# Optimization experiments

Measured on AMD Instinct MI355X. Metric: run time of the kernel, lower is better.

The kernel has to match this reference:

```python
import jax, jax.numpy as jnp
import numpy as np

B, C, L, H = 8, 1024, 1024, 16
DK = C // H
SCALE = 1.0 / np.sqrt(DK)


def setup_inputs() -> dict:
    key = jax.random.key(0)
    ks = jax.random.split(key, 9)
    s = 1.0 / np.sqrt(C)
    return {
        "q": jax.random.normal(ks[0], (B, C, L), dtype=jnp.float32),
        "k": jax.random.normal(ks[1], (B, C, L), dtype=jnp.float32),
        "v": jax.random.normal(ks[2], (B, C, L), dtype=jnp.float32),
        "Wq": jax.random.normal(ks[3], (C, C), dtype=jnp.float32) * s,
        "bq": jax.random.normal(ks[4], (C,), dtype=jnp.float32) * s,
        "Wk": jax.random.normal(ks[5], (C, C), dtype=jnp.float32) * s,
        "bk": jax.random.normal(ks[6], (C,), dtype=jnp.float32) * s,
        "Wv": jax.random.normal(ks[7], (C, C), dtype=jnp.float32) * s,
        "bv": jax.random.normal(ks[8], (C,), dtype=jnp.float32) * s,
    }


def _proj(x, W, b):
    # Conv1d kernel_size=1 == pointwise linear over channels: (b,c,l) -> (b,o,l)
    return jnp.einsum('oc,bcl->bol', W, x) + b[None, :, None]


def reference(q, k, v, Wq, bq, Wk, bk, Wv, bv):
    b = q.shape[0]
    qh = _proj(q, Wq, bq).reshape(b * H, DK, L)
    kh = _proj(k, Wk, bk).reshape(b * H, DK, L)
    vh = _proj(v, Wv, bv).reshape(b * H, DK, L)
    # scores[bh, t, s] = sum_c q[bh,c,t] k[bh,c,s]
    scores = jnp.einsum('bct,bcs->bts', qh, kh) * SCALE
    # NOTE: original uses nn.Softmax(dim=1) -> softmax over the query axis t
    attn = jax.nn.softmax(scores, axis=1)
    # dropout is identity in eval / p=0
    out = jnp.einsum('bts,bcs->bct', attn, vh)  # (b*H, d_k, L)
    return out.reshape(b, C, L)
```

## Files before the change

### kernel.cpp

```cpp
#include <hip/hip_runtime.h>
#include <stdint.h>

typedef unsigned short ushort_t;
typedef float  f32x4  __attribute__((ext_vector_type(4)));
typedef short  short8 __attribute__((ext_vector_type(8)));
typedef short  short4v __attribute__((ext_vector_type(4)));

#define QSCALE 0.18033688011112043f

__device__ __forceinline__ ushort_t f2bf(float f) {
  unsigned u = __builtin_bit_cast(unsigned, f);
  unsigned r = (u + 0x7fffu + ((u >> 16) & 1u)) >> 16;
  return (ushort_t)r;
}
__device__ __forceinline__ float bf2f(ushort_t u) {
  unsigned x = (unsigned)u << 16;
  return __builtin_bit_cast(float, x);
}

typedef const __attribute__((address_space(1))) unsigned int* gas_t;
typedef __attribute__((address_space(3))) unsigned int* las_t;
__device__ __forceinline__ void gload16(const void* g, void* l) {
  __builtin_amdgcn_global_load_lds((gas_t)g, (las_t)l, 16, 0, 0);
}

__global__ __launch_bounds__(256) void transpose_cvt3(
    const float* __restrict__ q, const float* __restrict__ k,
    const float* __restrict__ v, ushort_t* __restrict__ oq,
    ushort_t* __restrict__ ok, ushort_t* __restrict__ ov) {
  __shared__ float tile[64][65];
  int z = blockIdx.z;
  int t = z >> 3, b = z & 7;
  const float* in = (t == 0) ? q : (t == 1) ? k : v;
  ushort_t* out = (t == 0) ? oq : (t == 1) ? ok : ov;
  int c0 = blockIdx.x * 64, l0 = blockIdx.y * 64;
  int col = threadIdx.x & 63;
  int row4 = threadIdx.x >> 6;
  const float* p = in + ((size_t)b * 1024 + c0) * 1024 + l0;
#pragma unroll
  for (int i = 0; i < 16; ++i) {
    int r = row4 * 16 + i;
    tile[r][col] = p[(size_t)r * 1024 + col];
  }
  __syncthreads();
  ushort_t* qo = out + ((size_t)b * 1024 + l0) * 1024 + c0;
#pragma unroll
  for (int i = 0; i < 16; ++i) {
    int r = row4 * 16 + i;
    qo[(size_t)r * 1024 + col] = f2bf(tile[col][r]);
  }
}

__global__ __launch_bounds__(256) void cvt_w3(
    const float* __restrict__ Wq, const float* __restrict__ Wk,
    const float* __restrict__ Wv, ushort_t* __restrict__ oq,
    ushort_t* __restrict__ ok, ushort_t* __restrict__ ov) {
  int seg = blockIdx.x >> 10;
  const float* in = (seg == 0) ? Wq : (seg == 1) ? Wk : Wv;
  ushort_t* out = (seg == 0) ? oq : (seg == 1) ? ok : ov;
  float sc = (seg == 0) ? QSCALE : 1.0f;
  int i = (blockIdx.x & 1023) * 256 + threadIdx.x;
  f32x4 v = *reinterpret_cast<const f32x4*>(in + (size_t)i * 4);
  short4v pk;
#pragma unroll
  for (int j = 0; j < 4; ++j) pk[j] = (short)f2bf(v[j] * sc);
  *reinterpret_cast<short4v*>(out + (size_t)i * 4) = pk;
}

template <bool OUT_T>
__global__ __launch_bounds__(256) void gemm_bt(const ushort_t* __restrict__ A,
                                               const ushort_t* __restrict__ BT,
                                               const float* __restrict__ bias,
                                               float bs,
                                               ushort_t* __restrict__ outp) {
  __shared__ ushort_t As[128 * 32];
  __shared__ ushort_t Bs[128 * 32];
  int b = blockIdx.z;
  int Mbase = blockIdx.y * 128, Nbase = blockIdx.x * 128;
  int tid = threadIdx.x;
  int lane = tid & 63, wave = tid >> 6;
  int wr = wave >> 1, wc = wave & 1;
  int lo = lane & 15, hi = lane >> 4;
  const ushort_t* Bb = BT + ((size_t)b << 20);

  f32x4 acc[4][4] = {};

  for (int kt = 0; kt < 1024; kt += 32) {
#pragma unroll
    for (int it = 0; it < 2; ++it) {
      int cch = tid + it * 256;
      int r = cch >> 2, p = cch & 3;
      gload16(A + (size_t)(Mbase + r) * 1024 + kt + p * 8, &As[it * 2048 + wave * 512]);
      gload16(Bb + (size_t)(Nbase + r) * 1024 + kt + p * 8, &Bs[it * 2048 + wave * 512]);
    }
    __syncthreads();
    short8 af[4], bf[4];
#pragma unroll
    for (int m = 0; m < 4; ++m)
      af[m] = *reinterpret_cast<const short8*>(&As[(wr * 64 + m * 16 + lo) * 32 + hi * 8]);
#pragma unroll
    for (int n = 0; n < 4; ++n)
      bf[n] = *reinterpret_cast<const short8*>(&Bs[(wc * 64 + n * 16 + lo) * 32 + hi * 8]);
#pragma unroll
    for (int m = 0; m < 4; ++m)
#pragma unroll
      for (int n = 0; n < 4; ++n)
        acc[m][n] = __builtin_amdgcn_mfma_f32_16x16x32_bf16(af[m], bf[n], acc[m][n], 0, 0, 0);
    __syncthreads();
  }

#pragma unroll
  for (int m = 0; m < 4; ++m) {
    int o0 = Mbase + wr * 64 + m * 16 + hi * 4;
#pragma unroll
    for (int n = 0; n < 4; ++n) {
      int col = Nbase + wc * 64 + n * 16 + lo;
      if (OUT_T) {
        short4v pk;
#pragma unroll
        for (int j = 0; j < 4; ++j) pk[j] = (short)f2bf(acc[m][n][j] + bias[o0 + j] * bs);
        *reinterpret_cast<short4v*>(outp + ((size_t)b << 20) + ((size_t)(o0 >> 6) << 16) +
                                    (size_t)col * 64 + (o0 & 63)) = pk;
      } else {
#pragma unroll
        for (int j = 0; j < 4; ++j)
          outp[((size_t)b << 20) + (size_t)(o0 + j) * 1024 + col] =
              f2bf(acc[m][n][j] + bias[o0 + j] * bs);
      }
    }
  }
}

__global__ __launch_bounds__(256) void attn_zs(const ushort_t* __restrict__ qhT,
                                               const ushort_t* __restrict__ khT,
                                               ushort_t* __restrict__ vhb) {
  __shared__ float zbuf[2][2][64];
  __shared__ float invs[128];
  int bid = blockIdx.y * 8 + blockIdx.x;
  int logical = (bid & 7) * 128 + (bid >> 3);
  int sblk = logical & 7, bh = logical >> 3;
  int tid = threadIdx.x;
  int lane = tid & 63, wave = tid >> 6;
  int wr = wave >> 1, wc = wave & 1;
  int lo = lane & 15, hi = lane >> 4;
  const ushort_t* kb = khT + ((size_t)bh << 16);
  const ushort_t* qb = qhT + ((size_t)bh << 16);

  int sbase = sblk * 128 + wr * 64;
  short8 af[4][2];
#pragma unroll
  for (int m = 0; m < 4; ++m)
#pragma unroll
    for (int kk = 0; kk < 2; ++kk)
      af[m][kk] = *reinterpret_cast<const short8*>(
          kb + (size_t)(sbase + m * 16 + lo) * 64 + kk * 32 + hi * 8);

  float zp[4][4] = {};

  for (int t0 = 0; t0 < 1024; t0 += 128) {
    int tbase = t0 + wc * 64;
    short8 bf[4][2];
#pragma unroll
    for (int n = 0; n < 4; ++n)
#pragma unroll
      for (int kk = 0; kk < 2; ++kk)
        bf[n][kk] = *reinterpret_cast<const short8*>(
            qb + (size_t)(tbase + n * 16 + lo) * 64 + kk * 32 + hi * 8);
#pragma unroll
    for (int m = 0; m < 4; ++m)
#pragma unroll
      for (int n = 0; n < 4; ++n) {
        f32x4 dd = {0.f, 0.f, 0.f, 0.f};
        __builtin_amdgcn_s_setprio(1);
        dd = __builtin_amdgcn_mfma_f32_16x16x32_bf16(af[m][0], bf[n][0], dd, 0, 0, 0);
        dd = __builtin_amdgcn_mfma_f32_16x16x32_bf16(af[m][1], bf[n][1], dd, 0, 0, 0);
        __builtin_amdgcn_s_setprio(0);
#pragma unroll
        for (int j = 0; j < 4; ++j) zp[m][j] += __builtin_amdgcn_exp2f(dd[j]);
      }
  }
#pragma unroll
  for (int m = 0; m < 4; ++m)
#pragma unroll
    for (int j = 0; j < 4; ++j) {
      float v = zp[m][j];
      v += __shfl_xor(v, 1);
      v += __shfl_xor(v, 2);
      v += __shfl_xor(v, 4);
      v += __shfl_xor(v, 8);
      if (lo == 0) zbuf[wc][wr][m * 16 + hi * 4 + j] = v;
    }
  __syncthreads();
  if (tid < 128)
    invs[tid] = 1.0f / (zbuf[0][tid >> 6][tid & 63] + zbuf[1][tid >> 6][tid & 63]);
  __syncthreads();

  int d = tid >> 2, soff = (tid & 3) * 32;
  ushort_t* vp = vhb + ((size_t)bh << 16) + (size_t)d * 1024 + sblk * 128 + soff;
#pragma unroll
  for (int c = 0; c < 4; ++c) {
    short8 vv = *reinterpret_cast<const short8*>(vp + c * 8);
    short8 o;
#pragma unroll
    for (int j = 0; j < 8; ++j)
      o[j] = (short)f2bf(bf2f((ushort_t)vv[j]) * invs[soff + c * 8 + j]);
    *reinterpret_cast<short8*>(vp + c * 8) = o;
  }
}

__global__ __launch_bounds__(256) void attn_av(const ushort_t* __restrict__ qhT,
                                               const ushort_t* __restrict__ khT,
                                               const ushort_t* __restrict__ vs,
                                               float* __restrict__ out) {
  __shared__ ushort_t Ks[2][64 * 64];
  __shared__ ushort_t Vt[2][64 * 64];
  __shared__ ushort_t Pt[4][32 * 64];
  int bid = blockIdx.y * 8 + blockIdx.x;
  int logical = (bid & 7) * 128 + (bid >> 3);
  int tblk = logical & 7, bh = logical >> 3;
  int tid = threadIdx.x;
  int lane = tid & 63, wave = tid >> 6;
  int lo = lane & 15, hi = lane >> 4;
  const ushort_t* qb = qhT + ((size_t)bh << 16);
  const char* kbase = (const char*)(khT + ((size_t)bh << 16));
  const char* vbase = (const char*)(vs + ((size_t)bh << 16));
  int t0 = tblk * 128 + wave * 32;

  short8 bq[2][2];
#pragma unroll
  for (int n = 0; n < 2; ++n)
#pragma unroll
    for (int kk = 0; kk < 2; ++kk)
      bq[n][kk] = *reinterpret_cast<const short8*>(
          qb + (size_t)(t0 + n * 16 + lo) * 64 + kk * 32 + hi * 8);

  f32x4 acc[4][2] = {};
  char* pw = (char*)Pt[wave];
  int swl = (lo & 7) << 4;

  auto stageKV = [&](int buf, int s0) {
#pragma unroll
    for (int r = 0; r < 2; ++r) {
      int L = r * 4096 + tid * 16;
      int row = L >> 7;
      int off = (L & 127) ^ ((row & 7) << 4);
      gload16(kbase + (size_t)(s0 + row) * 128 + off,
              (char*)Ks + buf * 8192 + r * 4096 + wave * 1024);
      gload16(vbase + (size_t)row * 2048 + (size_t)s0 * 2 + off,
              (char*)Vt + buf * 8192 + r * 4096 + wave * 1024);
    }
  };

  auto computeTile = [&](int buf) {
    char* ksb = (char*)Ks + buf * 8192;
    char* vtb = (char*)Vt + buf * 8192;
#pragma unroll
    for (int m = 0; m < 4; ++m) {
      int srow = m * 16 + lo;
      int sws = (srow & 7) << 4;
      short8 af0 = *reinterpret_cast<const short8*>(ksb + srow * 128 + ((hi * 16) ^ sws));
      short8 af1 = *reinterpret_cast<const short8*>(ksb + srow * 128 + ((64 + hi * 16) ^ sws));
#pragma unroll
      for (int n = 0; n < 2; ++n) {
        f32x4 dd = {0.f, 0.f, 0.f, 0.f};
        __builtin_amdgcn_s_setprio(1);
        dd = __builtin_amdgcn_mfma_f32_16x16x32_bf16(af0, bq[n][0], dd, 0, 0, 0);
        dd = __builtin_amdgcn_mfma_f32_16x16x32_bf16(af1, bq[n][1], dd, 0, 0, 0);
        __builtin_amdgcn_s_setprio(0);
        short4v pk;
#pragma unroll
        for (int j = 0; j < 4; ++j) pk[j] = (short)f2bf(__builtin_amdgcn_exp2f(dd[j]));
        *reinterpret_cast<short4v*>(
            pw + (n * 16 + lo) * 128 + ((m * 32 + hi * 8) ^ swl)) = pk;
      }
    }
    asm volatile("s_waitcnt lgkmcnt(0)" ::: "memory");
    __builtin_amdgcn_sched_barrier(0);

    short8 bp[2][2];
#pragma unroll
    for (int n = 0; n < 2; ++n)
#pragma unroll
      for (int kk = 0; kk < 2; ++kk)
        bp[n][kk] = *reinterpret_cast<const short8*>(
            pw + (n * 16 + lo) * 128 + ((kk * 64 + hi * 16) ^ swl));
    __builtin_amdgcn_s_setprio(1);
#pragma unroll
    for (int m = 0; m < 4; ++m) {
      int drow = m * 16 + lo;
      int swd = (drow & 7) << 4;
      short8 av0 = *reinterpret_cast<const short8*>(vtb + drow * 128 + ((hi * 16) ^ swd));
      short8 av1 = *reinterpret_cast<const short8*>(vtb + drow * 128 + ((64 + hi * 16) ^ swd));
#pragma unroll
      for (int n = 0; n < 2; ++n) {
        acc[m][n] = __builtin_amdgcn_mfma_f32_16x16x32_bf16(av0, bp[n][0], acc[m][n], 0, 0, 0);
        acc[m][n] = __builtin_amdgcn_mfma_f32_16x16x32_bf16(av1, bp[n][1], acc[m][n], 0, 0, 0);
      }
    }
    __builtin_amdgcn_s_setprio(0);
  };

  stageKV(0, 0);
#pragma unroll 1
  for (int i = 0; i < 15; ++i) {
    stageKV((i + 1) & 1, (i + 1) * 64);
    asm volatile("s_waitcnt vmcnt(4)" ::: "memory");
    __builtin_amdgcn_s_barrier();
    __builtin_amdgcn_sched_barrier(0);
    computeTile(i & 1);
    __builtin_amdgcn_s_barrier();
  }
  asm volatile("s_waitcnt vmcnt(0)" ::: "memory");
  __builtin_amdgcn_s_barrier();
  __builtin_amdgcn_sched_barrier(0);
  computeTile(1);

  float* ob = out + ((size_t)bh << 16);
#pragma unroll
  for (int m = 0; m < 4; ++m)
#pragma unroll
    for (int n = 0; n < 2; ++n)
#pragma unroll
      for (int j = 0; j < 4; ++j)
        ob[(size_t)(m * 16 + hi * 4 + j) * 1024 + t0 + n * 16 + lo] = acc[m][n][j];
}

extern "C" void kernel_launch(void* const* d_in, const int* in_sizes, int n_in,
                              void* d_out, int out_size, void* d_ws, size_t ws_size,
                              hipStream_t stream) {
  const float* q  = (const float*)d_in[0];
  const float* k  = (const float*)d_in[1];
  const float* v  = (const float*)d_in[2];
  const float* Wq = (const float*)d_in[3];
  const float* bq = (const float*)d_in[4];
  const float* Wk = (const float*)d_in[5];
  const float* bk = (const float*)d_in[6];
  const float* Wv = (const float*)d_in[7];
  const float* bv = (const float*)d_in[8];
  float* out = (float*)d_out;
  char* ws = (char*)d_ws;
  const size_t MB = 1u << 20;

  ushort_t* xTq = (ushort_t*)(ws);
  ushort_t* xTk = (ushort_t*)(ws + 16 * MB);
  ushort_t* xTv = (ushort_t*)(ws + 32 * MB);
  ushort_t* Wqb = (ushort_t*)(ws + 48 * MB);
  ushort_t* Wkb = (ushort_t*)(ws + 50 * MB);
  ushort_t* Wvb = (ushort_t*)(ws + 52 * MB);
  ushort_t* qhT = (ushort_t*)(ws + 54 * MB);
  ushort_t* khT = xTq;
  ushort_t* vhb = xTk;

  dim3 tb(256);
  transpose_cvt3<<<dim3(16, 16, 24), tb, 0, stream>>>(q, k, v, xTq, xTk, xTv);
  cvt_w3<<<dim3(3072), tb, 0, stream>>>(Wq, Wk, Wv, Wqb, Wkb, Wvb);
  gemm_bt<true ><<<dim3(8, 8, 8), tb, 0, stream>>>(Wqb, xTq, bq, QSCALE, qhT);
  gemm_bt<true ><<<dim3(8, 8, 8), tb, 0, stream>>>(Wkb, xTk, bk, 1.0f, khT);
  gemm_bt<false><<<dim3(8, 8, 8), tb, 0, stream>>>(Wvb, xTv, bv, 1.0f, vhb);
  attn_zs<<<dim3(8, 128), tb, 0, stream>>>(qhT, khT, vhb);
  attn_av<<<dim3(8, 128), tb, 0, stream>>>(qhT, khT, vhb, out);
}
```

Before: 333.6 us.

## Remap GEMM grid to 1D batch-interleaved, drop setprio and KV double-buffering

The projection GEMMs now launch as a flat 1D grid whose block index is decoded so consecutive blocks land on different batches. The attention kernels drop the s_setprio hints around MFMA groups. attn_av replaces its double-buffered K/V staging, with explicit vmcnt waits and barriers, by a single-buffer load, __syncthreads, compute, __syncthreads loop. This halves shared memory, which may allow more resident blocks, but the global loads no longer overlap with compute.

```diff
diff --git a/kernel.cpp b/kernel.cpp
--- a/kernel.cpp
+++ b/kernel.cpp
@@ -75,8 +75,10 @@
                                                ushort_t* __restrict__ outp) {
   __shared__ ushort_t As[128 * 32];
   __shared__ ushort_t Bs[128 * 32];
-  int b = blockIdx.z;
-  int Mbase = blockIdx.y * 128, Nbase = blockIdx.x * 128;
+  int bid = blockIdx.x;
+  int b = bid & 7;
+  int within = bid >> 3;
+  int Mbase = (within >> 3) * 128, Nbase = (within & 7) * 128;
   int tid = threadIdx.x;
   int lane = tid & 63, wave = tid >> 6;
   int wr = wave >> 1, wc = wave & 1;
@@ -171,10 +173,8 @@
 #pragma unroll
       for (int n = 0; n < 4; ++n) {
         f32x4 dd = {0.f, 0.f, 0.f, 0.f};
-        __builtin_amdgcn_s_setprio(1);
         dd = __builtin_amdgcn_mfma_f32_16x16x32_bf16(af[m][0], bf[n][0], dd, 0, 0, 0);
         dd = __builtin_amdgcn_mfma_f32_16x16x32_bf16(af[m][1], bf[n][1], dd, 0, 0, 0);
-        __builtin_amdgcn_s_setprio(0);
 #pragma unroll
         for (int j = 0; j < 4; ++j) zp[m][j] += __builtin_amdgcn_exp2f(dd[j]);
       }
@@ -212,8 +212,8 @@
                                                const ushort_t* __restrict__ khT,
                                                const ushort_t* __restrict__ vs,
                                                float* __restrict__ out) {
-  __shared__ ushort_t Ks[2][64 * 64];
-  __shared__ ushort_t Vt[2][64 * 64];
+  __shared__ ushort_t Ks[64 * 64];
+  __shared__ ushort_t Vt[64 * 64];
   __shared__ ushort_t Pt[4][32 * 64];
   int bid = blockIdx.y * 8 + blockIdx.x;
   int logical = (bid & 7) * 128 + (bid >> 3);
@@ -238,35 +238,32 @@
   char* pw = (char*)Pt[wave];
   int swl = (lo & 7) << 4;
 
-  auto stageKV = [&](int buf, int s0) {
+  for (int s0 = 0; s0 < 1024; s0 += 64) {
 #pragma unroll
     for (int r = 0; r < 2; ++r) {
       int L = r * 4096 + tid * 16;
       int row = L >> 7;
       int off = (L & 127) ^ ((row & 7) << 4);
       gload16(kbase + (size_t)(s0 + row) * 128 + off,
-              (char*)Ks + buf * 8192 + r * 4096 + wave * 1024);
+              (char*)Ks + r * 4096 + wave * 1024);
       gload16(vbase + (size_t)row * 2048 + (size_t)s0 * 2 + off,
-              (char*)Vt + buf * 8192 + r * 4096 + wave * 1024);
-    }
-  };
-
-  auto computeTile = [&](int buf) {
-    char* ksb = (char*)Ks + buf * 8192;
-    char* vtb = (char*)Vt + buf * 8192;
+              (char*)Vt + r * 4096 + wave * 1024);
+    }
+    __syncthreads();
+
 #pragma unroll
     for (int m = 0; m < 4; ++m) {
       int srow = m * 16 + lo;
       int sws = (srow & 7) << 4;
-      short8 af0 = *reinterpret_cast<const short8*>(ksb + srow * 128 + ((hi * 16) ^ sws));
-      short8 af1 = *reinterpret_cast<const short8*>(ksb + srow * 128 + ((64 + hi * 16) ^ sws));
+      short8 af0 = *reinterpret_cast<const short8*>(
+          (char*)Ks + srow * 128 + ((hi * 16) ^ sws));
+      short8 af1 = *reinterpret_cast<const short8*>(
+          (char*)Ks + srow * 128 + ((64 + hi * 16) ^ sws));
 #pragma unroll
       for (int n = 0; n < 2; ++n) {
         f32x4 dd = {0.f, 0.f, 0.f, 0.f};
-        __builtin_amdgcn_s_setprio(1);
         dd = __builtin_amdgcn_mfma_f32_16x16x32_bf16(af0, bq[n][0], dd, 0, 0, 0);
         dd = __builtin_amdgcn_mfma_f32_16x16x32_bf16(af1, bq[n][1], dd, 0, 0, 0);
-        __builtin_amdgcn_s_setprio(0);
         short4v pk;
 #pragma unroll
         for (int j = 0; j < 4; ++j) pk[j] = (short)f2bf(__builtin_amdgcn_exp2f(dd[j]));
@@ -284,36 +281,22 @@
       for (int kk = 0; kk < 2; ++kk)
         bp[n][kk] = *reinterpret_cast<const short8*>(
             pw + (n * 16 + lo) * 128 + ((kk * 64 + hi * 16) ^ swl));
-    __builtin_amdgcn_s_setprio(1);
 #pragma unroll
     for (int m = 0; m < 4; ++m) {
       int drow = m * 16 + lo;
       int swd = (drow & 7) << 4;
-      short8 av0 = *reinterpret_cast<const short8*>(vtb + drow * 128 + ((hi * 16) ^ swd));
-      short8 av1 = *reinterpret_cast<const short8*>(vtb + drow * 128 + ((64 + hi * 16) ^ swd));
+      short8 av0 = *reinterpret_cast<const short8*>(
+          (char*)Vt + drow * 128 + ((hi * 16) ^ swd));
+      short8 av1 = *reinterpret_cast<const short8*>(
+          (char*)Vt + drow * 128 + ((64 + hi * 16) ^ swd));
 #pragma unroll
       for (int n = 0; n < 2; ++n) {
         acc[m][n] = __builtin_amdgcn_mfma_f32_16x16x32_bf16(av0, bp[n][0], acc[m][n], 0, 0, 0);
         acc[m][n] = __builtin_amdgcn_mfma_f32_16x16x32_bf16(av1, bp[n][1], acc[m][n], 0, 0, 0);
       }
     }
-    __builtin_amdgcn_s_setprio(0);
-  };
-
-  stageKV(0, 0);
-#pragma unroll 1
-  for (int i = 0; i < 15; ++i) {
-    stageKV((i + 1) & 1, (i + 1) * 64);
-    asm volatile("s_waitcnt vmcnt(4)" ::: "memory");
-    __builtin_amdgcn_s_barrier();
-    __builtin_amdgcn_sched_barrier(0);
-    computeTile(i & 1);
-    __builtin_amdgcn_s_barrier();
-  }
-  asm volatile("s_waitcnt vmcnt(0)" ::: "memory");
-  __builtin_amdgcn_s_barrier();
-  __builtin_amdgcn_sched_barrier(0);
-  computeTile(1);
+    __syncthreads();
+  }
 
   float* ob = out + ((size_t)bh << 16);
 #pragma unroll
@@ -354,9 +337,9 @@
   dim3 tb(256);
   transpose_cvt3<<<dim3(16, 16, 24), tb, 0, stream>>>(q, k, v, xTq, xTk, xTv);
   cvt_w3<<<dim3(3072), tb, 0, stream>>>(Wq, Wk, Wv, Wqb, Wkb, Wvb);
-  gemm_bt<true ><<<dim3(8, 8, 8), tb, 0, stream>>>(Wqb, xTq, bq, QSCALE, qhT);
-  gemm_bt<true ><<<dim3(8, 8, 8), tb, 0, stream>>>(Wkb, xTk, bk, 1.0f, khT);
-  gemm_bt<false><<<dim3(8, 8, 8), tb, 0, stream>>>(Wvb, xTv, bv, 1.0f, vhb);
+  gemm_bt<true ><<<dim3(512), tb, 0, stream>>>(Wqb, xTq, bq, QSCALE, qhT);
+  gemm_bt<true ><<<dim3(512), tb, 0, stream>>>(Wkb, xTk, bk, 1.0f, khT);
+  gemm_bt<false><<<dim3(512), tb, 0, stream>>>(Wvb, xTv, bv, 1.0f, vhb);
   attn_zs<<<dim3(8, 128), tb, 0, stream>>>(qhT, khT, vhb);
   attn_av<<<dim3(8, 128), tb, 0, stream>>>(qhT, khT, vhb, out);
 }
```

After: 329.0 us. About the same (-1.4%).
